# Performance work log

Measured on AMD Instinct MI355X. Metric: run time of the kernel, lower is better.

## Reference

```python
import jax, jax.numpy as jnp
import numpy as np

IN_FEATS = 512
OUT_FEATS = 512


def _xavier(key, shape, gain):
    fan_in, fan_out = shape[1], shape[0]
    a = gain * np.sqrt(6.0 / (fan_in + fan_out))
    return jax.random.uniform(key, shape, jnp.float32, -a, a)


def setup_inputs() -> dict:
    key = jax.random.key(0)
    ks = jax.random.split(key, 8)
    num_dst, num_vir, num_src = 8192, 32768, 131072
    n_e0, n_e1 = 524288, 131072
    gain = np.sqrt(2.0)  # calculate_gain('relu')
    feat = jax.random.normal(ks[0], (num_dst + num_src, IN_FEATS), jnp.float32)
    W_self = _xavier(ks[1], (OUT_FEATS, IN_FEATS), gain)
    b_self = jnp.zeros((OUT_FEATS,), jnp.float32)
    W_neigh = _xavier(ks[2], (OUT_FEATS, IN_FEATS), gain)
    e0_src = jax.random.randint(ks[3], (n_e0,), 0, num_src, jnp.int64 if jax.config.jax_enable_x64 else jnp.int32)
    e0_dst = jax.random.randint(ks[4], (n_e0,), 0, num_vir, e0_src.dtype)
    e1_src = jax.random.randint(ks[5], (n_e1,), 0, num_vir, e0_src.dtype)
    e1_dst = jax.random.randint(ks[6], (n_e1,), 0, num_dst, e0_src.dtype)
    return {
        "feat": feat, "W_self": W_self, "b_self": b_self, "W_neigh": W_neigh,
        "e0_src": e0_src, "e0_dst": e0_dst, "e1_src": e1_src, "e1_dst": e1_dst,
        "num_dst": num_dst, "num_vir": num_vir,
    }


def _seg_mean(msgs, dst, n):
    # DGL fn.mean: mean over incoming edges; zero-in-degree nodes get 0.
    s = jax.ops.segment_sum(msgs, dst, num_segments=n)
    c = jax.ops.segment_sum(jnp.ones((dst.shape[0], 1), msgs.dtype), dst, num_segments=n)
    return s / jnp.maximum(c, 1.0)


def reference(feat, W_self, b_self, W_neigh, e0_src, e0_dst, e1_src, e1_dst, num_dst, num_vir):
    # feat_drop is identity (p=0.0)
    h_dst = feat[:num_dst] @ W_self.T + b_self              # [num_dst, out]
    feat_src = feat[num_dst:]                                # [num_src, in]
    h_src = feat_src @ W_neigh.T                             # [num_src, out]
    # block0: copy_u + mean -> virtual nodes
    h_vir = _seg_mean(h_src[e0_src], e0_dst, num_vir)        # [num_vir, out]
    # SPFeatureShuffle is identity in single-partition setting
    # block1: copy_u + mean -> dst nodes
    h_neigh = _seg_mean(h_vir[e1_src], e1_dst, num_dst)      # [num_dst, out]
    rst = h_dst + h_neigh                                    # activation=None, norm=None
    return rst
```

## Files before the change

### kernel.cpp

```cpp
#include <hip/hip_runtime.h>
#include <hip/hip_bf16.h>
#include <stdint.h>

#define NUM_DST 8192
#define NUM_VIR 32768
#define F       512

typedef short bf16x8 __attribute__((ext_vector_type(8)));
typedef float f32x4  __attribute__((ext_vector_type(4)));

__device__ __forceinline__ unsigned short f2bf(float f) {
  union { float f; unsigned int u; } v; v.f = f;
  unsigned int u = v.u;
  unsigned int r = (u + 0x7fffu + ((u >> 16) & 1u)) >> 16;
  return (unsigned short)r;
}
__device__ __forceinline__ float bf2f(unsigned int hbits) {
  union { unsigned int u; float f; } v; v.u = hbits << 16;
  return v.f;
}

__global__ void rank_kernel(const int* __restrict__ dst, int ne,
                            int* __restrict__ counts, int* __restrict__ ranks) {
  int i = blockIdx.x * blockDim.x + threadIdx.x;
  if (i < ne) ranks[i] = atomicAdd(&counts[dst[i]], 1);
}

__global__ void scan_kernel(const int* __restrict__ counts, int* __restrict__ offs, int n) {
  __shared__ int part[1024];
  int t = threadIdx.x;
  int chunk = n >> 10;
  int base = t * chunk;
  int s = 0;
  for (int i = 0; i < chunk; ++i) s += counts[base + i];
  part[t] = s;
  __syncthreads();
  for (int d = 1; d < 1024; d <<= 1) {
    int v = (t >= d) ? part[t - d] : 0;
    __syncthreads();
    part[t] += v;
    __syncthreads();
  }
  int run = part[t] - s;
  for (int i = 0; i < chunk; ++i) { offs[base + i] = run; run += counts[base + i]; }
  if (t == 1023) offs[n] = run;
}

__global__ void scatter_kernel(const int* __restrict__ src, const int* __restrict__ dst,
                               const int* __restrict__ ranks, const int* __restrict__ offs,
                               int* __restrict__ sorted, int ne) {
  int i = blockIdx.x * blockDim.x + threadIdx.x;
  if (i < ne) sorted[offs[dst[i]] + ranks[i]] = src[i];
}

__global__ void agg0_kernel(const float* __restrict__ feat, const int* __restrict__ sorted,
                            const int* __restrict__ offs, unsigned int* __restrict__ fvir) {
  int b = blockIdx.x, t = threadIdx.x;
  int s0 = offs[b], s1 = offs[b + 1];
  const float* base = feat + (size_t)NUM_DST * F;
  float a0 = 0.f, a1 = 0.f, a2 = 0.f, a3 = 0.f;
  for (int i = s0; i < s1; ++i) {
    int src = sorted[i];
    const float4* rp = (const float4*)(base + (size_t)src * F);
    float4 v = rp[t];
    a0 += v.x; a1 += v.y; a2 += v.z; a3 += v.w;
  }
  int c = s1 - s0; if (c < 1) c = 1;
  float inv = 1.0f / (float)c;
  unsigned int p0 = (unsigned int)f2bf(a0 * inv) | ((unsigned int)f2bf(a1 * inv) << 16);
  unsigned int p1 = (unsigned int)f2bf(a2 * inv) | ((unsigned int)f2bf(a3 * inv) << 16);
  uint2* op = (uint2*)(fvir + (size_t)b * (F / 2));
  op[t] = make_uint2(p0, p1);
}

__global__ void agg1_kernel(const unsigned int* __restrict__ fvir, const int* __restrict__ sorted,
                            const int* __restrict__ offs, unsigned int* __restrict__ a2out) {
  int b = blockIdx.x, t = threadIdx.x;
  int s0 = offs[b], s1 = offs[b + 1];
  float a0 = 0.f, a1 = 0.f, a2 = 0.f, a3 = 0.f;
  for (int i = s0; i < s1; ++i) {
    int v = sorted[i];
    const uint2* rp = (const uint2*)(fvir + (size_t)v * (F / 2));
    uint2 u = rp[t];
    a0 += bf2f(u.x & 0xffffu); a1 += bf2f(u.x >> 16);
    a2 += bf2f(u.y & 0xffffu); a3 += bf2f(u.y >> 16);
  }
  int c = s1 - s0; if (c < 1) c = 1;
  float inv = 1.0f / (float)c;
  unsigned int p0 = (unsigned int)f2bf(a0 * inv) | ((unsigned int)f2bf(a1 * inv) << 16);
  unsigned int p1 = (unsigned int)f2bf(a2 * inv) | ((unsigned int)f2bf(a3 * inv) << 16);
  uint2* op = (uint2*)(a2out + (size_t)b * (F / 2));
  op[t] = make_uint2(p0, p1);
}

__global__ void conv_a1_kernel(const float* __restrict__ feat, uint2* __restrict__ a1) {
  int i = blockIdx.x * blockDim.x + threadIdx.x;
  float4 v = ((const float4*)feat)[i];
  unsigned int p0 = (unsigned int)f2bf(v.x) | ((unsigned int)f2bf(v.y) << 16);
  unsigned int p1 = (unsigned int)f2bf(v.z) | ((unsigned int)f2bf(v.w) << 16);
  a1[i] = make_uint2(p0, p1);
}

__global__ void conv_w_kernel(const float* __restrict__ Wself, const float* __restrict__ Wneigh,
                              unsigned short* __restrict__ wcat) {
  int i = blockIdx.x * blockDim.x + threadIdx.x;
  int n = i >> 10, k = i & 1023;
  float w = (k < F) ? Wself[(n << 9) + k] : Wneigh[(n << 9) + (k - F)];
  wcat[i] = f2bf(w);
}

__global__ __launch_bounds__(256) void gemm_kernel(
    const unsigned short* __restrict__ A1, const unsigned short* __restrict__ A2,
    const unsigned short* __restrict__ W, const float* __restrict__ bias,
    float* __restrict__ out) {
  __shared__ unsigned short As[128 * 72];
  __shared__ unsigned short Bs[64 * 72];
  int t = threadIdx.x;
  int lane = t & 63, wid = t >> 6;
  int wm = wid & 1, wn = wid >> 1;
  int l16 = lane & 15, quad = lane >> 4;
  int m0 = blockIdx.x * 128, n0 = blockIdx.y * 64;

  f32x4 acc[4][2];
  for (int fi = 0; fi < 4; ++fi)
    for (int ni = 0; ni < 2; ++ni)
      acc[fi][ni] = (f32x4){0.f, 0.f, 0.f, 0.f};

  for (int kt = 0; kt < 16; ++kt) {
    const unsigned short* Asrc = (kt < 8) ? A1 : A2;
    int kk0 = (kt & 7) * 64;
#pragma unroll
    for (int r = 0; r < 4; ++r) {
      int q = r * 256 + t;
      int row = q >> 3, c = q & 7;
      uint4 v = *(const uint4*)(Asrc + (size_t)(m0 + row) * F + kk0 + c * 8);
      *(uint4*)(&As[row * 72 + c * 8]) = v;
    }
#pragma unroll
    for (int r = 0; r < 2; ++r) {
      int q = r * 256 + t;
      int row = q >> 3, c = q & 7;
      uint4 v = *(const uint4*)(W + (size_t)(n0 + row) * 1024 + kt * 64 + c * 8);
      *(uint4*)(&Bs[row * 72 + c * 8]) = v;
    }
    __syncthreads();
#pragma unroll
    for (int kk = 0; kk < 2; ++kk) {
      bf16x8 a[4], b[2];
#pragma unroll
      for (int fi = 0; fi < 4; ++fi)
        a[fi] = *(const bf16x8*)(&As[(wm * 64 + fi * 16 + l16) * 72 + kk * 32 + quad * 8]);
#pragma unroll
      for (int ni = 0; ni < 2; ++ni)
        b[ni] = *(const bf16x8*)(&Bs[(wn * 32 + ni * 16 + l16) * 72 + kk * 32 + quad * 8]);
#pragma unroll
      for (int fi = 0; fi < 4; ++fi)
#pragma unroll
        for (int ni = 0; ni < 2; ++ni)
          acc[fi][ni] = __builtin_amdgcn_mfma_f32_16x16x32_bf16(a[fi], b[ni], acc[fi][ni], 0, 0, 0);
    }
    __syncthreads();
  }
#pragma unroll
  for (int ni = 0; ni < 2; ++ni) {
    int n = n0 + wn * 32 + ni * 16 + l16;
    float bv = bias[n];
#pragma unroll
    for (int fi = 0; fi < 4; ++fi) {
#pragma unroll
      for (int reg = 0; reg < 4; ++reg) {
        int m = m0 + wm * 64 + fi * 16 + quad * 4 + reg;
        out[(size_t)m * F + n] = acc[fi][ni][reg] + bv;
      }
    }
  }
}

extern "C" void kernel_launch(void* const* d_in, const int* in_sizes, int n_in,
                              void* d_out, int out_size, void* d_ws, size_t ws_size,
                              hipStream_t stream) {
  const float* feat    = (const float*)d_in[0];
  const float* W_self  = (const float*)d_in[1];
  const float* b_self  = (const float*)d_in[2];
  const float* W_neigh = (const float*)d_in[3];
  const int*   e0_src  = (const int*)d_in[4];
  const int*   e0_dst  = (const int*)d_in[5];
  const int*   e1_src  = (const int*)d_in[6];
  const int*   e1_dst  = (const int*)d_in[7];
  int ne0 = in_sizes[4];
  int ne1 = in_sizes[6];

  char* ws = (char*)d_ws;
  size_t off = 0;
  auto nxt = [&](size_t bytes) -> char* {
    char* p = ws + off;
    off += (bytes + 255) & ~(size_t)255;
    return p;
  };
  int* counts0 = (int*)nxt((size_t)NUM_VIR * 4);
  int* counts1 = (int*)nxt((size_t)NUM_DST * 4);
  int* offs0   = (int*)nxt(((size_t)NUM_VIR + 1) * 4);
  int* offs1   = (int*)nxt(((size_t)NUM_DST + 1) * 4);
  int* ranks0  = (int*)nxt((size_t)ne0 * 4);
  int* sorted0 = (int*)nxt((size_t)ne0 * 4);
  int* ranks1  = (int*)nxt((size_t)ne1 * 4);
  int* sorted1 = (int*)nxt((size_t)ne1 * 4);
  unsigned int*   fvir = (unsigned int*)nxt((size_t)NUM_VIR * F * 2);
  unsigned short* a1   = (unsigned short*)nxt((size_t)NUM_DST * F * 2);
  unsigned short* a2   = (unsigned short*)nxt((size_t)NUM_DST * F * 2);
  unsigned short* wcat = (unsigned short*)nxt((size_t)F * 1024 * 2);
  (void)ws_size;

  hipMemsetAsync(counts0, 0, (size_t)(NUM_VIR + NUM_DST) * 4, stream);

  rank_kernel<<<(ne0 + 255) / 256, 256, 0, stream>>>(e0_dst, ne0, counts0, ranks0);
  rank_kernel<<<(ne1 + 255) / 256, 256, 0, stream>>>(e1_dst, ne1, counts1, ranks1);
  scan_kernel<<<1, 1024, 0, stream>>>(counts0, offs0, NUM_VIR);
  scan_kernel<<<1, 1024, 0, stream>>>(counts1, offs1, NUM_DST);
  scatter_kernel<<<(ne0 + 255) / 256, 256, 0, stream>>>(e0_src, e0_dst, ranks0, offs0, sorted0, ne0);
  scatter_kernel<<<(ne1 + 255) / 256, 256, 0, stream>>>(e1_src, e1_dst, ranks1, offs1, sorted1, ne1);

  agg0_kernel<<<NUM_VIR, 128, 0, stream>>>(feat, sorted0, offs0, fvir);
  agg1_kernel<<<NUM_DST, 128, 0, stream>>>(fvir, sorted1, offs1, (unsigned int*)a2);

  conv_a1_kernel<<<(NUM_DST * F / 4) / 256, 256, 0, stream>>>(feat, (uint2*)a1);
  conv_w_kernel<<<(F * 1024) / 256, 256, 0, stream>>>(W_self, W_neigh, wcat);

  dim3 ggrid(NUM_DST / 128, F / 64);
  gemm_kernel<<<ggrid, 256, 0, stream>>>(a1, a2, wcat, b_self, (float*)d_out);
}
```

Before: 638.5 us.

## Pre-convert features to bf16 and gather bf16 rows; merge small preprocessing kernels

Converts the full feature matrix to bf16 once, when workspace allows, so the edge-0 aggregation gathers half-width rows instead of fp32 rows. Aggregation now uses one wavefront per segment with 16-byte loads per lane. The rank, scan, scatter and conversion kernels are merged to cut launch count. The trade-off is an extra full streaming pass over the features, and the path depends on workspace size.

```diff
diff --git a/kernel.cpp b/kernel.cpp
--- a/kernel.cpp
+++ b/kernel.cpp
@@ -1,9 +1,9 @@
 #include <hip/hip_runtime.h>
-#include <hip/hip_bf16.h>
 #include <stdint.h>
 
 #define NUM_DST 8192
 #define NUM_VIR 32768
+#define NUM_SRC 131072
 #define F       512
 
 typedef short bf16x8 __attribute__((ext_vector_type(8)));
@@ -15,18 +15,34 @@
   unsigned int r = (u + 0x7fffu + ((u >> 16) & 1u)) >> 16;
   return (unsigned short)r;
 }
-__device__ __forceinline__ float bf2f(unsigned int hbits) {
-  union { unsigned int u; float f; } v; v.u = hbits << 16;
-  return v.f;
-}
-
-__global__ void rank_kernel(const int* __restrict__ dst, int ne,
-                            int* __restrict__ counts, int* __restrict__ ranks) {
+__device__ __forceinline__ unsigned int pack2(float a, float b) {
+  return (unsigned int)f2bf(a) | ((unsigned int)f2bf(b) << 16);
+}
+__device__ __forceinline__ float lo2f(unsigned int u) {
+  union { unsigned int u; float f; } v; v.u = u << 16; return v.f;
+}
+__device__ __forceinline__ float hi2f(unsigned int u) {
+  union { unsigned int u; float f; } v; v.u = u & 0xffff0000u; return v.f;
+}
+
+__global__ void rank_all(const int* __restrict__ e0d, int ne0,
+                         const int* __restrict__ e1d, int ne1,
+                         int* __restrict__ c0, int* __restrict__ c1,
+                         int* __restrict__ r0, int* __restrict__ r1) {
   int i = blockIdx.x * blockDim.x + threadIdx.x;
-  if (i < ne) ranks[i] = atomicAdd(&counts[dst[i]], 1);
-}
-
-__global__ void scan_kernel(const int* __restrict__ counts, int* __restrict__ offs, int n) {
+  if (i < ne0) {
+    r0[i] = atomicAdd(&c0[e0d[i]], 1);
+  } else {
+    int j = i - ne0;
+    if (j < ne1) r1[j] = atomicAdd(&c1[e1d[j]], 1);
+  }
+}
+
+__global__ void scan_all(const int* __restrict__ c0, int* __restrict__ o0, int n0,
+                         const int* __restrict__ c1, int* __restrict__ o1, int n1) {
+  const int* counts = (blockIdx.x == 0) ? c0 : c1;
+  int* offs         = (blockIdx.x == 0) ? o0 : o1;
+  int n             = (blockIdx.x == 0) ? n0 : n1;
   __shared__ int part[1024];
   int t = threadIdx.x;
   int chunk = n >> 10;
@@ -46,67 +62,90 @@
   if (t == 1023) offs[n] = run;
 }
 
-__global__ void scatter_kernel(const int* __restrict__ src, const int* __restrict__ dst,
-                               const int* __restrict__ ranks, const int* __restrict__ offs,
-                               int* __restrict__ sorted, int ne) {
+__global__ void scatter_all(const int* __restrict__ e0s, const int* __restrict__ e0d,
+                            const int* __restrict__ r0, const int* __restrict__ o0,
+                            int* __restrict__ sorted0, int ne0,
+                            const int* __restrict__ e1s, const int* __restrict__ e1d,
+                            const int* __restrict__ r1, const int* __restrict__ o1,
+                            int* __restrict__ sorted1, int ne1) {
   int i = blockIdx.x * blockDim.x + threadIdx.x;
-  if (i < ne) sorted[offs[dst[i]] + ranks[i]] = src[i];
-}
-
-__global__ void agg0_kernel(const float* __restrict__ feat, const int* __restrict__ sorted,
-                            const int* __restrict__ offs, unsigned int* __restrict__ fvir) {
+  if (i < ne0) {
+    sorted0[o0[e0d[i]] + r0[i]] = e0s[i];
+  } else {
+    int j = i - ne0;
+    if (j < ne1) sorted1[o1[e1d[j]] + r1[j]] = e1s[j];
+  }
+}
+
+__global__ void convert_all(const float* __restrict__ feat,
+                            const float* __restrict__ Wself, const float* __restrict__ Wneigh,
+                            uint4* __restrict__ fbf, unsigned short* __restrict__ wcat,
+                            int featBlocks) {
   int b = blockIdx.x, t = threadIdx.x;
-  int s0 = offs[b], s1 = offs[b + 1];
-  const float* base = feat + (size_t)NUM_DST * F;
-  float a0 = 0.f, a1 = 0.f, a2 = 0.f, a3 = 0.f;
+  if (b < featBlocks) {
+    size_t tid = (size_t)b * 256 + t;
+    const float4* fp = (const float4*)feat;
+    float4 v0 = fp[tid * 2], v1 = fp[tid * 2 + 1];
+    uint4 o;
+    o.x = pack2(v0.x, v0.y); o.y = pack2(v0.z, v0.w);
+    o.z = pack2(v1.x, v1.y); o.w = pack2(v1.z, v1.w);
+    fbf[tid] = o;
+  } else {
+    int idx = (b - featBlocks) * 256 + t;
+    int n = idx >> 7, kb = (idx & 127) * 8;
+    const float* src = (kb < F) ? (Wself + (size_t)n * F + kb)
+                                : (Wneigh + (size_t)n * F + (kb - F));
+    float4 v0 = *(const float4*)src;
+    float4 v1 = *(const float4*)(src + 4);
+    uint4 o;
+    o.x = pack2(v0.x, v0.y); o.y = pack2(v0.z, v0.w);
+    o.z = pack2(v1.x, v1.y); o.w = pack2(v1.z, v1.w);
+    *(uint4*)(wcat + (size_t)n * 1024 + kb) = o;
+  }
+}
+
+__global__ void agg_bf16(const uint4* __restrict__ table, const int* __restrict__ sorted,
+                         const int* __restrict__ offs, uint4* __restrict__ outbf) {
+  int seg  = blockIdx.x * 4 + (threadIdx.x >> 6);
+  int lane = threadIdx.x & 63;
+  int s0 = offs[seg], s1 = offs[seg + 1];
+  float a0 = 0.f, a1 = 0.f, a2 = 0.f, a3 = 0.f, a4 = 0.f, a5 = 0.f, a6 = 0.f, a7 = 0.f;
   for (int i = s0; i < s1; ++i) {
     int src = sorted[i];
-    const float4* rp = (const float4*)(base + (size_t)src * F);
-    float4 v = rp[t];
-    a0 += v.x; a1 += v.y; a2 += v.z; a3 += v.w;
+    uint4 u = table[(size_t)src * 64 + lane];
+    a0 += lo2f(u.x); a1 += hi2f(u.x);
+    a2 += lo2f(u.y); a3 += hi2f(u.y);
+    a4 += lo2f(u.z); a5 += hi2f(u.z);
+    a6 += lo2f(u.w); a7 += hi2f(u.w);
   }
   int c = s1 - s0; if (c < 1) c = 1;
   float inv = 1.0f / (float)c;
-  unsigned int p0 = (unsigned int)f2bf(a0 * inv) | ((unsigned int)f2bf(a1 * inv) << 16);
-  unsigned int p1 = (unsigned int)f2bf(a2 * inv) | ((unsigned int)f2bf(a3 * inv) << 16);
-  uint2* op = (uint2*)(fvir + (size_t)b * (F / 2));
-  op[t] = make_uint2(p0, p1);
-}
-
-__global__ void agg1_kernel(const unsigned int* __restrict__ fvir, const int* __restrict__ sorted,
-                            const int* __restrict__ offs, unsigned int* __restrict__ a2out) {
-  int b = blockIdx.x, t = threadIdx.x;
-  int s0 = offs[b], s1 = offs[b + 1];
-  float a0 = 0.f, a1 = 0.f, a2 = 0.f, a3 = 0.f;
+  uint4 o;
+  o.x = pack2(a0 * inv, a1 * inv); o.y = pack2(a2 * inv, a3 * inv);
+  o.z = pack2(a4 * inv, a5 * inv); o.w = pack2(a6 * inv, a7 * inv);
+  outbf[(size_t)seg * 64 + lane] = o;
+}
+
+__global__ void agg0_f32(const float* __restrict__ feat, const int* __restrict__ sorted,
+                         const int* __restrict__ offs, uint4* __restrict__ outbf) {
+  int seg  = blockIdx.x * 4 + (threadIdx.x >> 6);
+  int lane = threadIdx.x & 63;
+  int s0 = offs[seg], s1 = offs[seg + 1];
+  const float4* base = (const float4*)(feat + (size_t)NUM_DST * F);
+  float a0 = 0.f, a1 = 0.f, a2 = 0.f, a3 = 0.f, a4 = 0.f, a5 = 0.f, a6 = 0.f, a7 = 0.f;
   for (int i = s0; i < s1; ++i) {
-    int v = sorted[i];
-    const uint2* rp = (const uint2*)(fvir + (size_t)v * (F / 2));
-    uint2 u = rp[t];
-    a0 += bf2f(u.x & 0xffffu); a1 += bf2f(u.x >> 16);
-    a2 += bf2f(u.y & 0xffffu); a3 += bf2f(u.y >> 16);
+    int src = sorted[i];
+    float4 v0 = base[(size_t)src * 128 + lane * 2];
+    float4 v1 = base[(size_t)src * 128 + lane * 2 + 1];
+    a0 += v0.x; a1 += v0.y; a2 += v0.z; a3 += v0.w;
+    a4 += v1.x; a5 += v1.y; a6 += v1.z; a7 += v1.w;
   }
   int c = s1 - s0; if (c < 1) c = 1;
   float inv = 1.0f / (float)c;
-  unsigned int p0 = (unsigned int)f2bf(a0 * inv) | ((unsigned int)f2bf(a1 * inv) << 16);
-  unsigned int p1 = (unsigned int)f2bf(a2 * inv) | ((unsigned int)f2bf(a3 * inv) << 16);
-  uint2* op = (uint2*)(a2out + (size_t)b * (F / 2));
-  op[t] = make_uint2(p0, p1);
-}
-
-__global__ void conv_a1_kernel(const float* __restrict__ feat, uint2* __restrict__ a1) {
-  int i = blockIdx.x * blockDim.x + threadIdx.x;
-  float4 v = ((const float4*)feat)[i];
-  unsigned int p0 = (unsigned int)f2bf(v.x) | ((unsigned int)f2bf(v.y) << 16);
-  unsigned int p1 = (unsigned int)f2bf(v.z) | ((unsigned int)f2bf(v.w) << 16);
-  a1[i] = make_uint2(p0, p1);
-}
-
-__global__ void conv_w_kernel(const float* __restrict__ Wself, const float* __restrict__ Wneigh,
-                              unsigned short* __restrict__ wcat) {
-  int i = blockIdx.x * blockDim.x + threadIdx.x;
-  int n = i >> 10, k = i & 1023;
-  float w = (k < F) ? Wself[(n << 9) + k] : Wneigh[(n << 9) + (k - F)];
-  wcat[i] = f2bf(w);
+  uint4 o;
+  o.x = pack2(a0 * inv, a1 * inv); o.y = pack2(a2 * inv, a3 * inv);
+  o.z = pack2(a4 * inv, a5 * inv); o.w = pack2(a6 * inv, a7 * inv);
+  outbf[(size_t)seg * 64 + lane] = o;
 }
 
 __global__ __launch_bounds__(256) void gemm_kernel(
@@ -205,27 +244,37 @@
   int* sorted0 = (int*)nxt((size_t)ne0 * 4);
   int* ranks1  = (int*)nxt((size_t)ne1 * 4);
   int* sorted1 = (int*)nxt((size_t)ne1 * 4);
-  unsigned int*   fvir = (unsigned int*)nxt((size_t)NUM_VIR * F * 2);
-  unsigned short* a1   = (unsigned short*)nxt((size_t)NUM_DST * F * 2);
-  unsigned short* a2   = (unsigned short*)nxt((size_t)NUM_DST * F * 2);
+  uint4* fvir  = (uint4*)nxt((size_t)NUM_VIR * F * 2);
+  uint4* a2    = (uint4*)nxt((size_t)NUM_DST * F * 2);
   unsigned short* wcat = (unsigned short*)nxt((size_t)F * 1024 * 2);
-  (void)ws_size;
+  size_t fixed = off;
+  size_t bigRows = (size_t)(NUM_DST + NUM_SRC);
+  size_t need_big = fixed + bigRows * F * 2;
+  bool big = (ws_size >= need_big);
+  size_t nrows = big ? bigRows : (size_t)NUM_DST;
+  uint4* fbf = (uint4*)nxt(nrows * F * 2);
 
   hipMemsetAsync(counts0, 0, (size_t)(NUM_VIR + NUM_DST) * 4, stream);
 
-  rank_kernel<<<(ne0 + 255) / 256, 256, 0, stream>>>(e0_dst, ne0, counts0, ranks0);
-  rank_kernel<<<(ne1 + 255) / 256, 256, 0, stream>>>(e1_dst, ne1, counts1, ranks1);
-  scan_kernel<<<1, 1024, 0, stream>>>(counts0, offs0, NUM_VIR);
-  scan_kernel<<<1, 1024, 0, stream>>>(counts1, offs1, NUM_DST);
-  scatter_kernel<<<(ne0 + 255) / 256, 256, 0, stream>>>(e0_src, e0_dst, ranks0, offs0, sorted0, ne0);
-  scatter_kernel<<<(ne1 + 255) / 256, 256, 0, stream>>>(e1_src, e1_dst, ranks1, offs1, sorted1, ne1);
-
-  agg0_kernel<<<NUM_VIR, 128, 0, stream>>>(feat, sorted0, offs0, fvir);
-  agg1_kernel<<<NUM_DST, 128, 0, stream>>>(fvir, sorted1, offs1, (unsigned int*)a2);
-
-  conv_a1_kernel<<<(NUM_DST * F / 4) / 256, 256, 0, stream>>>(feat, (uint2*)a1);
-  conv_w_kernel<<<(F * 1024) / 256, 256, 0, stream>>>(W_self, W_neigh, wcat);
+  int neTot = ne0 + ne1;
+  rank_all<<<(neTot + 255) / 256, 256, 0, stream>>>(e0_dst, ne0, e1_dst, ne1,
+                                                    counts0, counts1, ranks0, ranks1);
+  scan_all<<<2, 1024, 0, stream>>>(counts0, offs0, NUM_VIR, counts1, offs1, NUM_DST);
+  scatter_all<<<(neTot + 255) / 256, 256, 0, stream>>>(
+      e0_src, e0_dst, ranks0, offs0, sorted0, ne0,
+      e1_src, e1_dst, ranks1, offs1, sorted1, ne1);
+
+  int featBlocks = (int)(nrows / 4);
+  convert_all<<<featBlocks + 256, 256, 0, stream>>>(feat, W_self, W_neigh, fbf, wcat, featBlocks);
+
+  if (big) {
+    agg_bf16<<<NUM_VIR / 4, 256, 0, stream>>>(fbf + (size_t)NUM_DST * 64, sorted0, offs0, fvir);
+  } else {
+    agg0_f32<<<NUM_VIR / 4, 256, 0, stream>>>(feat, sorted0, offs0, fvir);
+  }
+  agg_bf16<<<NUM_DST / 4, 256, 0, stream>>>(fvir, sorted1, offs1, a2);
 
   dim3 ggrid(NUM_DST / 128, F / 64);
-  gemm_kernel<<<ggrid, 256, 0, stream>>>(a1, a2, wcat, b_self, (float*)d_out);
-}
+  gemm_kernel<<<ggrid, 256, 0, stream>>>((const unsigned short*)fbf, (const unsigned short*)a2,
+                                         wcat, b_self, (float*)d_out);
+}
```

After: 635.0 us. Within noise of the previous version (-0.5%).
